# Optimization experiments

Hardware: AMD Instinct MI355X
Metric: run time of the kernel (lower is better)

## Reference

```python
import jax, jax.numpy as jnp
import numpy as np

B, IC, HW = 16, 32, 128
NF, OC, K, GROUP = 8, 64, 5, 8


def _rotate_filters(w, theta):
    """Bilinear rotation of filters w [N, C, k, k] by angle theta.
    Matches torch affine_grid + grid_sample (align_corners=False, zero padding)."""
    k = w.shape[-1]
    base = (2.0 * jnp.arange(k, dtype=w.dtype) + 1.0) / k - 1.0  # pixel-center normalized coords
    ys, xs = jnp.meshgrid(base, base, indexing='ij')  # [k, k]
    c, s = jnp.cos(theta), jnp.sin(theta)
    # sampling grid = rot_mat @ [x, y, 1]
    gx = c * xs - s * ys
    gy = s * xs + c * ys
    # normalized -> pixel coords (align_corners=False)
    ix = ((gx + 1.0) * k - 1.0) / 2.0
    iy = ((gy + 1.0) * k - 1.0) / 2.0
    x0 = jnp.floor(ix)
    y0 = jnp.floor(iy)
    wx1 = ix - x0
    wy1 = iy - y0
    wx0 = 1.0 - wx1
    wy0 = 1.0 - wy1

    def gather(yy, xx):
        valid = ((xx >= 0) & (xx < k) & (yy >= 0) & (yy < k)).astype(w.dtype)
        xc = jnp.clip(xx, 0, k - 1).astype(jnp.int32)
        yc = jnp.clip(yy, 0, k - 1).astype(jnp.int32)
        return w[:, :, yc, xc] * valid  # [N, C, k, k]

    return (gather(y0, x0) * (wy0 * wx0)
            + gather(y0, x0 + 1.0) * (wy0 * wx1)
            + gather(y0 + 1.0, x0) * (wy1 * wx0)
            + gather(y0 + 1.0, x0 + 1.0) * (wy1 * wx1))


def _forward(x, kernel, relaxed_weights):
    nf, oc, ic, k, _ = kernel.shape
    group = relaxed_weights.shape[1]
    wflat = kernel.reshape(nf * oc, ic, k, k)
    thetas = -2.0 * jnp.pi / group * jnp.arange(group, dtype=x.dtype)
    # [group, nf*oc, ic, k, k]
    fb = jax.vmap(lambda t: _rotate_filters(wflat, t))(thetas)
    # -> [nf, oc, group, ic, k, k]
    fb = jnp.transpose(fb, (1, 0, 2, 3, 4)).reshape(nf, oc, group, ic, k, k)
    w = jnp.einsum('na,noaikl->oaikl', relaxed_weights, fb)
    w = w.reshape(oc * group, ic, k, k)
    pad = (k - 1) // 2
    y = jax.lax.conv_general_dilated(
        x, w, window_strides=(1, 1), padding=[(pad, pad), (pad, pad)],
        dimension_numbers=('NCHW', 'OIHW', 'NCHW'))
    b, _, h, wd = y.shape
    y = y.reshape(b, oc, group, wd, h)  # matches torch .view(B, O, A, W, H)
    return jax.nn.leaky_relu(y, negative_slope=0.01)


def setup_inputs() -> dict:
    key = jax.random.key(0)
    k1, k2, k3 = jax.random.split(key, 3)
    x = jax.random.normal(k1, (B, IC, HW, HW), dtype=jnp.float32)
    kernel = jax.random.normal(k2, (NF, OC, IC, K, K), dtype=jnp.float32) * 0.05
    relaxed_weights = jax.random.normal(k3, (NF, GROUP), dtype=jnp.float32)
    return {"x": x, "kernel": kernel, "relaxed_weights": relaxed_weights}


def reference(x, kernel, relaxed_weights):
    return _forward(x, kernel, relaxed_weights)
```

## Files before the change

### kernel.cpp

```cpp
#include <hip/hip_runtime.h>
#include <hip/hip_bf16.h>
#include <math.h>

#define B_   16
#define IC_  32
#define HW_  128
#define NF_  8
#define OC_  64
#define K_   5
#define GRP_ 8
#define COTOT_ (OC_ * GRP_)
#define XTH  132
#define TAPSTRIDE (COTOT_ * IC_)
#define XROWB (XTH * IC_ * 2)
#define HW2  (HW_ * HW_)

typedef short  short8  __attribute__((ext_vector_type(8)));
typedef unsigned short ushort8 __attribute__((ext_vector_type(8)));
typedef float  f32x4   __attribute__((ext_vector_type(4)));

static __device__ inline unsigned short f2bf(float f) {
    unsigned u = __builtin_bit_cast(unsigned, f);
    unsigned r = (u + 0x7FFFu + ((u >> 16) & 1u)) >> 16;
    return (unsigned short)r;
}

__device__ __forceinline__ void gload16(void* lds, const void* g) {
    __builtin_amdgcn_global_load_lds(
        (const __attribute__((address_space(1))) unsigned int*)g,
        (__attribute__((address_space(3))) unsigned int*)lds, 16, 0, 0);
}

__global__ __launch_bounds__(256) void xform_kernel(
    const float* __restrict__ x, unsigned short* __restrict__ xt) {
    int idx = blockIdx.x * blockDim.x + threadIdx.x;
    const int TOT = B_ * XTH * XTH;
    if (idx >= TOT) return;
    int wp = idx % XTH;
    int t  = idx / XTH;
    int hp = t % XTH;
    int b  = t / XTH;

    unsigned short vals[IC_];
    bool interior = (hp >= 2) && (hp < 2 + HW_) && (wp >= 2) && (wp < 2 + HW_);
    if (interior) {
        const float* xb = x + ((size_t)b * IC_) * HW2 + (hp - 2) * HW_ + (wp - 2);
        #pragma unroll
        for (int ic = 0; ic < IC_; ++ic)
            vals[ic] = f2bf(xb[(size_t)ic * HW2]);
    } else {
        #pragma unroll
        for (int ic = 0; ic < IC_; ++ic) vals[ic] = 0;
    }
    ushort8* dst = (ushort8*)(xt + (size_t)idx * IC_);
    #pragma unroll
    for (int c = 0; c < 4; ++c) {
        ushort8 v;
        #pragma unroll
        for (int j = 0; j < 8; ++j) v[j] = vals[c * 8 + j];
        dst[c] = v;
    }
}

__global__ __launch_bounds__(256) void build_w_kernel(
    const float* __restrict__ kern,
    const float* __restrict__ relaxed,
    unsigned short* __restrict__ wt) {
    int idx = blockIdx.x * blockDim.x + threadIdx.x;
    const int TOT = 25 * COTOT_ * IC_;
    if (idx >= TOT) return;
    int ic = idx & (IC_ - 1);
    int t  = idx >> 5;
    int co = t & (COTOT_ - 1);
    int e  = t >> 9;
    int a  = co & (GRP_ - 1);
    int o  = co >> 3;
    int i  = e / K_;
    int j  = e - i * K_;

    float theta = -6.283185307179586f / (float)GRP_ * (float)a;
    float cth = cosf(theta), sth = sinf(theta);
    float bx = (2.0f * (float)j + 1.0f) / (float)K_ - 1.0f;
    float by = (2.0f * (float)i + 1.0f) / (float)K_ - 1.0f;
    float gx = cth * bx - sth * by;
    float gy = sth * bx + cth * by;
    float ix = ((gx + 1.0f) * (float)K_ - 1.0f) * 0.5f;
    float iy = ((gy + 1.0f) * (float)K_ - 1.0f) * 0.5f;
    float x0 = floorf(ix), y0 = floorf(iy);
    float wx1 = ix - x0, wy1 = iy - y0;
    float wx0 = 1.0f - wx1, wy0 = 1.0f - wy1;

    float xs2[2]  = {x0, x0 + 1.0f};
    float ys2[2]  = {y0, y0 + 1.0f};
    float wxs[2] = {wx0, wx1};
    float wys[2] = {wy0, wy1};

    float tw[4];
    int   tyc[4], txc[4];
    #pragma unroll
    for (int dy = 0; dy < 2; ++dy) {
        #pragma unroll
        for (int dx = 0; dx < 2; ++dx) {
            float xx = xs2[dx], yy = ys2[dy];
            bool valid = (xx >= 0.0f) && (xx < (float)K_) &&
                         (yy >= 0.0f) && (yy < (float)K_);
            int tp = dy * 2 + dx;
            tw[tp]  = wys[dy] * wxs[dx] * (valid ? 1.0f : 0.0f);
            txc[tp] = (int)fminf(fmaxf(xx, 0.0f), (float)(K_ - 1));
            tyc[tp] = (int)fminf(fmaxf(yy, 0.0f), (float)(K_ - 1));
        }
    }

    float acc = 0.0f;
    #pragma unroll
    for (int n = 0; n < NF_; ++n) {
        const float* kb = kern + ((size_t)((n * OC_ + o) * IC_ + ic)) * (K_ * K_);
        float v = 0.0f;
        #pragma unroll
        for (int tp = 0; tp < 4; ++tp)
            v += kb[tyc[tp] * K_ + txc[tp]] * tw[tp];
        acc += relaxed[n * GRP_ + a] * v;
    }
    wt[idx] = f2bf(acc);
}

#define PREF_AF(dst, tap) {                                                   \
    const unsigned short* wp_ = wl + (size_t)(tap) * TAPSTRIDE;               \
    _Pragma("unroll")                                                         \
    for (int m = 0; m < 4; ++m)                                               \
        dst[m] = *(const short8*)(wp_ + (size_t)m * 16 * IC_);                \
}

#define COMP_JIT(afx) {                                                       \
    int base_ = prow + (pkx + l15) * 64 +                                     \
                ((l4 ^ (((pkx + l15) & 7) >> 1)) << 4);                       \
    short8 bf[8];                                                             \
    _Pragma("unroll")                                                         \
    for (int n = 0; n < 8; ++n)                                               \
        bf[n] = *(const short8*)(xsb + base_ + n * 1024);                     \
    __builtin_amdgcn_s_setprio(1);                                            \
    _Pragma("unroll")                                                         \
    for (int m = 0; m < 4; ++m)                                               \
        _Pragma("unroll")                                                     \
        for (int n = 0; n < 8; ++n)                                           \
            acc[m][n] = __builtin_amdgcn_mfma_f32_16x16x32_bf16(              \
                afx[m], bf[n], acc[m][n], 0, 0, 0);                           \
    __builtin_amdgcn_s_setprio(0);                                            \
    if (++pkx == 5) { pkx = 0; prow += XROWB; }                               \
}

__global__ __launch_bounds__(256, 2) void conv_mfma_kernel(
    const unsigned short* __restrict__ xt,
    const unsigned short* __restrict__ wt,
    float* __restrict__ out) {
    __shared__ __align__(16) unsigned short xs[8 * XTH * IC_];

    int tid  = threadIdx.x;
    int lane = tid & 63;
    int wv   = tid >> 6;
    int l15  = lane & 15;
    int l4   = lane >> 4;

    int hp = blockIdx.x;
    int b  = blockIdx.y;
    int cg = blockIdx.z;
    int cobase = cg * 64;
    int h0 = hp * 4;

    {
        const unsigned short* xb = xt + (((size_t)b * XTH + h0) * XTH) * IC_;
        #pragma unroll
        for (int i = 0; i < 17; ++i) {
            int sl = i * 256 + tid;
            if (sl < 4224) {
                int row = sl / 528;
                int rem = sl - row * 528;
                int w   = rem >> 2;
                int p   = rem & 3;
                int c   = p ^ ((w >> 1) & 3);
                gload16(&xs[sl * 8], xb + row * (XTH * IC_) + w * 32 + c * 8);
            }
        }
    }

    const unsigned short* wl = wt + (size_t)(cobase + l15) * IC_ + l4 * 8;
    const char* xsb = (const char*)xs;

    short8 afA[4], afB[4];
    PREF_AF(afA, 0);

    f32x4 acc[4][8];
    #pragma unroll
    for (int m = 0; m < 4; ++m)
        #pragma unroll
        for (int n = 0; n < 8; ++n) acc[m][n] = (f32x4)(0.0f);

    __syncthreads();

    int pkx  = 0;
    int prow = wv * XROWB;

    #pragma unroll 1
    for (int pi = 0; pi < 12; ++pi) {
        int t0 = pi * 2;
        PREF_AF(afB, t0 + 1);
        COMP_JIT(afA);
        PREF_AF(afA, t0 + 2);
        COMP_JIT(afB);
    }
    COMP_JIT(afA);

    int h = h0 + wv;
    float* ob = out + ((size_t)b * COTOT_ + cobase) * HW2 + (size_t)h * HW_;
    #pragma unroll
    for (int m = 0; m < 4; ++m) {
        #pragma unroll
        for (int n = 0; n < 8; ++n) {
            #pragma unroll
            for (int r = 0; r < 4; ++r) {
                int co = m * 16 + l4 * 4 + r;
                int w  = n * 16 + l15;
                float v = acc[m][n][r];
                v = fmaxf(v, 0.01f * v);
                ob[(size_t)co * HW2 + w] = v;
            }
        }
    }
}

extern "C" void kernel_launch(void* const* d_in, const int* in_sizes, int n_in,
                              void* d_out, int out_size, void* d_ws, size_t ws_size,
                              hipStream_t stream) {
    const float* x       = (const float*)d_in[0];
    const float* kernel  = (const float*)d_in[1];
    const float* relaxed = (const float*)d_in[2];
    float* out = (float*)d_out;

    unsigned short* xt = (unsigned short*)d_ws;
    unsigned short* wt = (unsigned short*)((char*)d_ws + (size_t)B_ * XTH * XTH * IC_ * 2);

    const int xtot = B_ * XTH * XTH;
    xform_kernel<<<(xtot + 255) / 256, 256, 0, stream>>>(x, xt);

    const int wtot = 25 * COTOT_ * IC_;
    build_w_kernel<<<(wtot + 255) / 256, 256, 0, stream>>>(kernel, relaxed, wt);

    dim3 grid(HW_ / 4, B_, COTOT_ / 64);
    conv_mfma_kernel<<<grid, 256, 0, stream>>>(xt, wt, out);
}
```

Measured before the change: 242.5 us.

## Fuse prep kernels and retile conv to 512-thread blocks with 256-channel groups

Merges the input-transform and weight-build kernels into one launch to drop a kernel boundary. The conv kernel moves to 512 threads per block covering 2 output rows and 256 output channels, with each wave computing 128 channels by 64 columns (8x4 MFMA tiles) instead of 64 channels by 128 columns. This shrinks the LDS input tile to 6 rows and changes the register-level reuse of weight versus input fragments. It also adds explicit barriers and waitcnts around each MFMA phase to keep waves in lockstep, which adds synchronisation cost and register pressure from the larger weight fragment arrays.

```diff
diff --git a/kernel.cpp b/kernel.cpp
--- a/kernel.cpp
+++ b/kernel.cpp
@@ -31,148 +31,152 @@
         (__attribute__((address_space(3))) unsigned int*)lds, 16, 0, 0);
 }
 
-__global__ __launch_bounds__(256) void xform_kernel(
-    const float* __restrict__ x, unsigned short* __restrict__ xt) {
-    int idx = blockIdx.x * blockDim.x + threadIdx.x;
-    const int TOT = B_ * XTH * XTH;
-    if (idx >= TOT) return;
-    int wp = idx % XTH;
-    int t  = idx / XTH;
-    int hp = t % XTH;
-    int b  = t / XTH;
-
-    unsigned short vals[IC_];
-    bool interior = (hp >= 2) && (hp < 2 + HW_) && (wp >= 2) && (wp < 2 + HW_);
-    if (interior) {
-        const float* xb = x + ((size_t)b * IC_) * HW2 + (hp - 2) * HW_ + (wp - 2);
-        #pragma unroll
-        for (int ic = 0; ic < IC_; ++ic)
-            vals[ic] = f2bf(xb[(size_t)ic * HW2]);
-    } else {
-        #pragma unroll
-        for (int ic = 0; ic < IC_; ++ic) vals[ic] = 0;
-    }
-    ushort8* dst = (ushort8*)(xt + (size_t)idx * IC_);
-    #pragma unroll
-    for (int c = 0; c < 4; ++c) {
-        ushort8 v;
-        #pragma unroll
-        for (int j = 0; j < 8; ++j) v[j] = vals[c * 8 + j];
-        dst[c] = v;
-    }
-}
-
-__global__ __launch_bounds__(256) void build_w_kernel(
+#define XFORM_BLOCKS 1089
+__global__ __launch_bounds__(256) void prep_kernel(
+    const float* __restrict__ x,
     const float* __restrict__ kern,
     const float* __restrict__ relaxed,
+    unsigned short* __restrict__ xt,
     unsigned short* __restrict__ wt) {
-    int idx = blockIdx.x * blockDim.x + threadIdx.x;
-    const int TOT = 25 * COTOT_ * IC_;
-    if (idx >= TOT) return;
-    int ic = idx & (IC_ - 1);
-    int t  = idx >> 5;
-    int co = t & (COTOT_ - 1);
-    int e  = t >> 9;
-    int a  = co & (GRP_ - 1);
-    int o  = co >> 3;
-    int i  = e / K_;
-    int j  = e - i * K_;
-
-    float theta = -6.283185307179586f / (float)GRP_ * (float)a;
-    float cth = cosf(theta), sth = sinf(theta);
-    float bx = (2.0f * (float)j + 1.0f) / (float)K_ - 1.0f;
-    float by = (2.0f * (float)i + 1.0f) / (float)K_ - 1.0f;
-    float gx = cth * bx - sth * by;
-    float gy = sth * bx + cth * by;
-    float ix = ((gx + 1.0f) * (float)K_ - 1.0f) * 0.5f;
-    float iy = ((gy + 1.0f) * (float)K_ - 1.0f) * 0.5f;
-    float x0 = floorf(ix), y0 = floorf(iy);
-    float wx1 = ix - x0, wy1 = iy - y0;
-    float wx0 = 1.0f - wx1, wy0 = 1.0f - wy1;
-
-    float xs2[2]  = {x0, x0 + 1.0f};
-    float ys2[2]  = {y0, y0 + 1.0f};
-    float wxs[2] = {wx0, wx1};
-    float wys[2] = {wy0, wy1};
-
-    float tw[4];
-    int   tyc[4], txc[4];
-    #pragma unroll
-    for (int dy = 0; dy < 2; ++dy) {
-        #pragma unroll
-        for (int dx = 0; dx < 2; ++dx) {
-            float xx = xs2[dx], yy = ys2[dy];
-            bool valid = (xx >= 0.0f) && (xx < (float)K_) &&
-                         (yy >= 0.0f) && (yy < (float)K_);
-            int tp = dy * 2 + dx;
-            tw[tp]  = wys[dy] * wxs[dx] * (valid ? 1.0f : 0.0f);
-            txc[tp] = (int)fminf(fmaxf(xx, 0.0f), (float)(K_ - 1));
-            tyc[tp] = (int)fminf(fmaxf(yy, 0.0f), (float)(K_ - 1));
-        }
-    }
-
-    float acc = 0.0f;
-    #pragma unroll
-    for (int n = 0; n < NF_; ++n) {
-        const float* kb = kern + ((size_t)((n * OC_ + o) * IC_ + ic)) * (K_ * K_);
-        float v = 0.0f;
-        #pragma unroll
-        for (int tp = 0; tp < 4; ++tp)
-            v += kb[tyc[tp] * K_ + txc[tp]] * tw[tp];
-        acc += relaxed[n * GRP_ + a] * v;
-    }
-    wt[idx] = f2bf(acc);
+    int tid = threadIdx.x;
+    if (blockIdx.x < XFORM_BLOCKS) {
+        int idx = blockIdx.x * 256 + tid;
+        int wp = idx % XTH;
+        int t  = idx / XTH;
+        int hp = t % XTH;
+        int b  = t / XTH;
+
+        unsigned short vals[IC_];
+        bool interior = (hp >= 2) && (hp < 2 + HW_) && (wp >= 2) && (wp < 2 + HW_);
+        if (interior) {
+            const float* xb = x + ((size_t)b * IC_) * HW2 + (hp - 2) * HW_ + (wp - 2);
+            #pragma unroll
+            for (int ic = 0; ic < IC_; ++ic)
+                vals[ic] = f2bf(xb[(size_t)ic * HW2]);
+        } else {
+            #pragma unroll
+            for (int ic = 0; ic < IC_; ++ic) vals[ic] = 0;
+        }
+        ushort8* dst = (ushort8*)(xt + (size_t)idx * IC_);
+        #pragma unroll
+        for (int c = 0; c < 4; ++c) {
+            ushort8 v;
+            #pragma unroll
+            for (int j = 0; j < 8; ++j) v[j] = vals[c * 8 + j];
+            dst[c] = v;
+        }
+    } else {
+        int idx = (blockIdx.x - XFORM_BLOCKS) * 256 + tid;
+        int ic = idx & (IC_ - 1);
+        int t  = idx >> 5;
+        int co = t & (COTOT_ - 1);
+        int e  = t >> 9;
+        int a  = co & (GRP_ - 1);
+        int o  = co >> 3;
+        int i  = e / K_;
+        int j  = e - i * K_;
+
+        float theta = -6.283185307179586f / (float)GRP_ * (float)a;
+        float cth = cosf(theta), sth = sinf(theta);
+        float bx = (2.0f * (float)j + 1.0f) / (float)K_ - 1.0f;
+        float by = (2.0f * (float)i + 1.0f) / (float)K_ - 1.0f;
+        float gx = cth * bx - sth * by;
+        float gy = sth * bx + cth * by;
+        float ix = ((gx + 1.0f) * (float)K_ - 1.0f) * 0.5f;
+        float iy = ((gy + 1.0f) * (float)K_ - 1.0f) * 0.5f;
+        float x0 = floorf(ix), y0 = floorf(iy);
+        float wx1 = ix - x0, wy1 = iy - y0;
+        float wx0 = 1.0f - wx1, wy0 = 1.0f - wy1;
+
+        float xs2[2]  = {x0, x0 + 1.0f};
+        float ys2[2]  = {y0, y0 + 1.0f};
+        float wxs[2] = {wx0, wx1};
+        float wys[2] = {wy0, wy1};
+
+        float tw[4];
+        int   tyc[4], txc[4];
+        #pragma unroll
+        for (int dy = 0; dy < 2; ++dy) {
+            #pragma unroll
+            for (int dx = 0; dx < 2; ++dx) {
+                float xx = xs2[dx], yy = ys2[dy];
+                bool valid = (xx >= 0.0f) && (xx < (float)K_) &&
+                             (yy >= 0.0f) && (yy < (float)K_);
+                int tp = dy * 2 + dx;
+                tw[tp]  = wys[dy] * wxs[dx] * (valid ? 1.0f : 0.0f);
+                txc[tp] = (int)fminf(fmaxf(xx, 0.0f), (float)(K_ - 1));
+                tyc[tp] = (int)fminf(fmaxf(yy, 0.0f), (float)(K_ - 1));
+            }
+        }
+
+        float acc = 0.0f;
+        #pragma unroll
+        for (int n = 0; n < NF_; ++n) {
+            const float* kb = kern + ((size_t)((n * OC_ + o) * IC_ + ic)) * (K_ * K_);
+            float v = 0.0f;
+            #pragma unroll
+            for (int tp = 0; tp < 4; ++tp)
+                v += kb[tyc[tp] * K_ + txc[tp]] * tw[tp];
+            acc += relaxed[n * GRP_ + a] * v;
+        }
+        wt[idx] = f2bf(acc);
+    }
 }
 
 #define PREF_AF(dst, tap) {                                                   \
     const unsigned short* wp_ = wl + (size_t)(tap) * TAPSTRIDE;               \
     _Pragma("unroll")                                                         \
-    for (int m = 0; m < 4; ++m)                                               \
+    for (int m = 0; m < 8; ++m)                                               \
         dst[m] = *(const short8*)(wp_ + (size_t)m * 16 * IC_);                \
 }
 
-#define COMP_JIT(afx) {                                                       \
-    int base_ = prow + (pkx + l15) * 64 +                                     \
+#define READ_BF() {                                                           \
+    int base_ = prow + (wq * 64 + pkx + l15) * 64 +                           \
                 ((l4 ^ (((pkx + l15) & 7) >> 1)) << 4);                       \
-    short8 bf[8];                                                             \
     _Pragma("unroll")                                                         \
-    for (int n = 0; n < 8; ++n)                                               \
+    for (int n = 0; n < 4; ++n)                                               \
         bf[n] = *(const short8*)(xsb + base_ + n * 1024);                     \
+    if (++pkx == 5) { pkx = 0; prow += XROWB; }                               \
+}
+
+#define MFMA32(afx) {                                                         \
     __builtin_amdgcn_s_setprio(1);                                            \
     _Pragma("unroll")                                                         \
-    for (int m = 0; m < 4; ++m)                                               \
+    for (int m = 0; m < 8; ++m)                                               \
         _Pragma("unroll")                                                     \
-        for (int n = 0; n < 8; ++n)                                           \
+        for (int n = 0; n < 4; ++n)                                           \
             acc[m][n] = __builtin_amdgcn_mfma_f32_16x16x32_bf16(              \
                 afx[m], bf[n], acc[m][n], 0, 0, 0);                           \
     __builtin_amdgcn_s_setprio(0);                                            \
-    if (++pkx == 5) { pkx = 0; prow += XROWB; }                               \
-}
-
-__global__ __launch_bounds__(256, 2) void conv_mfma_kernel(
+}
+
+__global__ __launch_bounds__(512, 2) void conv_mfma_kernel(
     const unsigned short* __restrict__ xt,
     const unsigned short* __restrict__ wt,
     float* __restrict__ out) {
-    __shared__ __align__(16) unsigned short xs[8 * XTH * IC_];
+    __shared__ __align__(16) unsigned short xs[6 * XTH * IC_];
 
     int tid  = threadIdx.x;
     int lane = tid & 63;
-    int wv   = tid >> 6;
+    int wid  = tid >> 6;
     int l15  = lane & 15;
     int l4   = lane >> 4;
+    int wr   = wid >> 2;
+    int hr   = (wid >> 1) & 1;
+    int wq   = wid & 1;
 
     int hp = blockIdx.x;
     int b  = blockIdx.y;
     int cg = blockIdx.z;
-    int cobase = cg * 64;
-    int h0 = hp * 4;
+    int cobase = cg * 256 + wr * 128;
+    int h0 = hp * 2;
 
     {
         const unsigned short* xb = xt + (((size_t)b * XTH + h0) * XTH) * IC_;
         #pragma unroll
-        for (int i = 0; i < 17; ++i) {
-            int sl = i * 256 + tid;
-            if (sl < 4224) {
+        for (int i = 0; i < 7; ++i) {
+            int sl = i * 512 + tid;
+            if (sl < 3168) {
                 int row = sl / 528;
                 int rem = sl - row * 528;
                 int w   = rem >> 2;
@@ -186,36 +190,49 @@
     const unsigned short* wl = wt + (size_t)(cobase + l15) * IC_ + l4 * 8;
     const char* xsb = (const char*)xs;
 
-    short8 afA[4], afB[4];
+    short8 afA[8], afB[8];
     PREF_AF(afA, 0);
 
-    f32x4 acc[4][8];
+    f32x4 acc[8][4];
     #pragma unroll
-    for (int m = 0; m < 4; ++m)
-        #pragma unroll
-        for (int n = 0; n < 8; ++n) acc[m][n] = (f32x4)(0.0f);
+    for (int m = 0; m < 8; ++m)
+        #pragma unroll
+        for (int n = 0; n < 4; ++n) acc[m][n] = (f32x4)(0.0f);
 
     __syncthreads();
 
     int pkx  = 0;
-    int prow = wv * XROWB;
+    int prow = hr * XROWB;
+    short8 bf[4];
 
     #pragma unroll 1
     for (int pi = 0; pi < 12; ++pi) {
         int t0 = pi * 2;
         PREF_AF(afB, t0 + 1);
-        COMP_JIT(afA);
+        READ_BF();
+        __builtin_amdgcn_s_barrier();
+        asm volatile("s_waitcnt vmcnt(8) lgkmcnt(0)" ::: "memory");
+        MFMA32(afA);
+        __builtin_amdgcn_s_barrier();
         PREF_AF(afA, t0 + 2);
-        COMP_JIT(afB);
-    }
-    COMP_JIT(afA);
-
-    int h = h0 + wv;
-    float* ob = out + ((size_t)b * COTOT_ + cobase) * HW2 + (size_t)h * HW_;
+        READ_BF();
+        __builtin_amdgcn_s_barrier();
+        asm volatile("s_waitcnt vmcnt(8) lgkmcnt(0)" ::: "memory");
+        MFMA32(afB);
+        __builtin_amdgcn_s_barrier();
+    }
+    READ_BF();
+    __builtin_amdgcn_s_barrier();
+    asm volatile("s_waitcnt vmcnt(0) lgkmcnt(0)" ::: "memory");
+    MFMA32(afA);
+
+    int h = h0 + hr;
+    float* ob = out + ((size_t)b * COTOT_ + cobase) * HW2
+                    + (size_t)h * HW_ + wq * 64;
     #pragma unroll
-    for (int m = 0; m < 4; ++m) {
-        #pragma unroll
-        for (int n = 0; n < 8; ++n) {
+    for (int m = 0; m < 8; ++m) {
+        #pragma unroll
+        for (int n = 0; n < 4; ++n) {
             #pragma unroll
             for (int r = 0; r < 4; ++r) {
                 int co = m * 16 + l4 * 4 + r;
@@ -239,12 +256,9 @@
     unsigned short* xt = (unsigned short*)d_ws;
     unsigned short* wt = (unsigned short*)((char*)d_ws + (size_t)B_ * XTH * XTH * IC_ * 2);
 
-    const int xtot = B_ * XTH * XTH;
-    xform_kernel<<<(xtot + 255) / 256, 256, 0, stream>>>(x, xt);
-
-    const int wtot = 25 * COTOT_ * IC_;
-    build_w_kernel<<<(wtot + 255) / 256, 256, 0, stream>>>(kernel, relaxed, wt);
-
-    dim3 grid(HW_ / 4, B_, COTOT_ / 64);
-    conv_mfma_kernel<<<grid, 256, 0, stream>>>(xt, wt, out);
-}
+    const int prep_blocks = XFORM_BLOCKS + (25 * COTOT_ * IC_) / 256;
+    prep_kernel<<<prep_blocks, 256, 0, stream>>>(x, kernel, relaxed, xt, wt);
+
+    dim3 grid(HW_ / 2, B_, COTOT_ / 256);
+    conv_mfma_kernel<<<grid, 512, 0, stream>>>(xt, wt, out);
+}
```

Measured after the change: 281.6 us. 16.1% more time.
